# Kernel optimization log

Measured on AMD Instinct MI355X. Metric: run time of the kernel, lower is better.

The kernel has to match this reference:

```python
import jax, jax.numpy as jnp
import numpy as np

N = 2000      # batch_size * num_rois
PS = 7        # pool_size
C = 256       # roi-align channels
HID = 1024    # head width
NC = 81       # num_classes (COCO incl. background)
EPS = 1e-3    # keras BatchNormalization default epsilon


def setup_inputs() -> dict:
    key = jax.random.key(0)
    ks = jax.random.split(key, 6)
    sc = lambda k, shape, s: jax.random.normal(k, shape, jnp.float32) * s
    return {
        "pooled_rois": jax.random.normal(ks[0], (N, PS, PS, C), jnp.float32),
        # 7x7 VALID conv on a 7x7 input == flattened dense: [PS*PS*C, HID]
        "w1": sc(ks[1], (PS * PS * C, HID), 0.01),
        "b1": jnp.zeros((HID,), jnp.float32),
        "gamma1": jnp.ones((HID,), jnp.float32),
        "beta1": jnp.zeros((HID,), jnp.float32),
        # 1x1 conv == dense [HID, HID]
        "w2": sc(ks[2], (HID, HID), 0.02),
        "b2": jnp.zeros((HID,), jnp.float32),
        "gamma2": jnp.ones((HID,), jnp.float32),
        "beta2": jnp.zeros((HID,), jnp.float32),
        "w_logits": sc(ks[3], (HID, NC), 0.02),
        "b_logits": jnp.zeros((NC,), jnp.float32),
        "w_delta": sc(ks[4], (HID, NC * 4), 0.02),
        "b_delta": jnp.zeros((NC * 4,), jnp.float32),
    }


def _batchnorm_train(x, gamma, beta):
    # training=True: normalize with batch statistics over the RoI axis
    mu = jnp.mean(x, axis=0)
    var = jnp.var(x, axis=0)
    return gamma * (x - mu) * jax.lax.rsqrt(var + EPS) + beta


def reference(pooled_rois, w1, b1, gamma1, beta1, w2, b2, gamma2, beta2,
              w_logits, b_logits, w_delta, b_delta):
    n = pooled_rois.shape[0]
    # rcnn_class_conv1: 7x7 VALID conv on 7x7 input -> flatten + matmul
    x = pooled_rois.reshape(n, -1) @ w1 + b1          # [N, 1024]
    x = jax.nn.relu(_batchnorm_train(x, gamma1, beta1))
    # rcnn_class_conv2: 1x1 conv -> matmul
    x = x @ w2 + b2                                    # [N, 1024]
    x = jax.nn.relu(_batchnorm_train(x, gamma2, beta2))
    logits = x @ w_logits + b_logits                   # [N, NC]
    probs = jax.nn.softmax(logits, axis=-1)            # [N, NC]
    deltas = (x @ w_delta + b_delta).reshape(n, NC, 4) # [N, NC, 4]
    return logits, probs, deltas
```

## Files before the change

### kernel.cpp

```cpp
#include <hip/hip_runtime.h>

typedef unsigned short u16;
typedef __bf16 bf16x8 __attribute__((ext_vector_type(8)));
typedef float f32x4 __attribute__((ext_vector_type(4)));
typedef u16 u16x8 __attribute__((ext_vector_type(8)));

static constexpr int kNRoi = 2000;
static constexpr int kMPad = 2048;
static constexpr int kKin  = 12544;
static constexpr int kHid  = 1024;
static constexpr int kNOutPad = 512;
static constexpr int kNC = 81;
static constexpr int kND = 324;


__device__ __forceinline__ u16 f2bf(float f) {
  union { float f; unsigned u; } v; v.f = f;
  unsigned r = v.u + 0x7fffu + ((v.u >> 16) & 1u);
  return (u16)(r >> 16);
}

__device__ __forceinline__ void transpose64(const float* __restrict__ in,
                                            u16* __restrict__ out, int R, int C,
                                            int bx, int by, u16* t, int tid) {
  const int cb = bx * 64, rb = by * 64;
  const int rl = tid >> 4, cl = (tid & 15) * 4;
#pragma unroll
  for (int i = 0; i < 4; ++i) {
    int r = rl + i * 16;
    f32x4 v = *(const f32x4*)(in + (long)(rb + r) * C + cb + cl);
#pragma unroll
    for (int j = 0; j < 4; ++j) t[(cl + j) * 72 + r] = f2bf(v[j]);
  }
  __syncthreads();
  const int c2 = tid >> 3, r2 = (tid & 7) * 8;
#pragma unroll
  for (int i = 0; i < 2; ++i) {
    int c = c2 + i * 32;
    u16x8 v = *(const u16x8*)&t[c * 72 + r2];
    *(u16x8*)(out + (long)(cb + c) * R + rb + r2) = v;
  }
}

__device__ __forceinline__ void transpose32(const float* __restrict__ in,
                                            u16* __restrict__ out, int R, int C,
                                            int bx, int by, u16* t, int tid) {
  int tx = tid & 31, ty = tid >> 5;
  int cb = bx * 32, rb = by * 32;
#pragma unroll
  for (int i = 0; i < 4; ++i) {
    int r = rb + ty + i * 8, c = cb + tx;
    if (r < R && c < C) t[(ty + i * 8) * 33 + tx] = f2bf(in[(long)r * C + c]);
  }
  __syncthreads();
#pragma unroll
  for (int i = 0; i < 4; ++i) {
    int c = cb + ty + i * 8, r = rb + tx;
    if (c < C && r < R) out[(long)c * R + r] = t[tx * 33 + ty + i * 8];
  }
}

__global__ __launch_bounds__(256) void prep(
    const float* __restrict__ w1, const float* __restrict__ w2,
    const float* __restrict__ wl, const float* __restrict__ wd,
    u16* __restrict__ W1T, u16* __restrict__ W2T, u16* __restrict__ WHT,
    float* __restrict__ S) {
  __shared__ u16 sh[64 * 72];
  const int tid = threadIdx.x;
  int id = blockIdx.x;
  if (id < 3136) { transpose64(w1, W1T, kKin, kHid, id & 15, id >> 4, sh, tid); return; }
  id -= 3136;
  if (id < 256)  { transpose64(w2, W2T, kHid, kHid, id & 15, id >> 4, sh, tid); return; }
  id -= 256;
  if (id < 96)   { transpose32(wl, WHT, kHid, kNC, id % 3, id / 3, sh, tid); return; }
  id -= 96;
  if (id < 352)  { transpose32(wd, WHT + kNC * kHid, kHid, kND, id % 11, id / 11, sh, tid); return; }
  id -= 352;
  if (id < 54) {
    int idx = id * 256 + tid;
    if (idx < 13696) *(u16x8*)(WHT + 405 * kHid + idx * 8) = (u16x8){};
    return;
  }
  id -= 54;
  *(f32x4*)(S + ((long)id * 256 + tid) * 4) = (f32x4){};
}

template<int AF32>
__global__ __launch_bounds__(256, 2) void gemm128(
    const float* __restrict__ Af, const u16* __restrict__ Ah,
    const u16* __restrict__ Bt, float* __restrict__ Cz, long zstride,
    int Mreal, int K, int N, int gy, int ntPer) {
  __shared__ u16 As[2][8192];
  __shared__ u16 Bs[2][8192];
  const int tid  = threadIdx.x;
  const int lane = tid & 63;
  const int w    = tid >> 6;
  const int wm   = (w >> 1) * 64;
  const int wn   = (w & 1) * 64;

  const int bl  = blockIdx.x;
  const int s   = bl >> 3;
  const int bx  = (bl & 7) * 2 + (s & 1);
  const int t2  = s >> 1;
  const int by  = t2 % gy;
  const int z   = t2 / gy;
  const long kb = (long)z * ntPer * 64;
  const int NT  = ntPer;

  const int rS = w * 8 + (lane >> 3);
  const int sg = (lane & 7) ^ ((lane >> 3) & 7);
  const u16* bp[4];
#pragma unroll
  for (int j = 0; j < 4; ++j)
    bp[j] = Bt + (long)(by * 128 + rS + j * 32) * K + kb + sg * 8;

  const u16* ap[4];
  const float* afp = nullptr;
  int rw = 0, hw = 0;
  if (AF32) {
    rw = tid >> 1; hw = tid & 1;
    long arow = (long)bx * 128 + rw; if (arow > Mreal - 1) arow = Mreal - 1;
    afp = Af + arow * K + kb + hw * 32;
  } else {
#pragma unroll
    for (int j = 0; j < 4; ++j) {
      long arow = (long)bx * 128 + rS + j * 32; if (arow > Mreal - 1) arow = Mreal - 1;
      ap[j] = Ah + arow * K + kb + sg * 8;
    }
  }

#define GLDS(p, dst) __builtin_amdgcn_global_load_lds( \
    (const __attribute__((address_space(1))) void*)(p), \
    (__attribute__((address_space(3))) void*)(dst), 16, 0, 0)
#define STG_B(b) do { _Pragma("unroll") for (int j_ = 0; j_ < 4; ++j_) { \
    GLDS(bp[j_], &Bs[b][j_ * 2048 + w * 512]); bp[j_] += 64; } } while (0)
#define STG_A(b) do { _Pragma("unroll") for (int j_ = 0; j_ < 4; ++j_) { \
    GLDS(ap[j_], &As[b][j_ * 2048 + w * 512]); ap[j_] += 64; } } while (0)

  f32x4 ar[8];
#define LDA32 do { _Pragma("unroll") for (int j_ = 0; j_ < 8; ++j_) \
    ar[j_] = *(const f32x4*)(afp + j_ * 4); afp += 64; } while (0)
#define WRA(b) do { _Pragma("unroll") for (int k_ = 0; k_ < 4; ++k_) { \
    u16x8 hh; _Pragma("unroll") for (int e_ = 0; e_ < 4; ++e_) { \
      hh[e_] = f2bf(ar[2 * k_][e_]); hh[4 + e_] = f2bf(ar[2 * k_ + 1][e_]); } \
    *(u16x8*)(&As[b][rw * 64 + ((hw * 4 + k_) ^ (rw & 7)) * 8]) = hh; } } while (0)

  const int fr = lane & 15;
  const int q  = lane >> 4;
  const int g0 = (q ^ (fr & 7)) * 8;
  const int g1 = ((q + 4) ^ (fr & 7)) * 8;

  f32x4 acc[4][4] = {};

#define LDFRAG(dst, base, off, gg) do { _Pragma("unroll") for (int i_ = 0; i_ < 4; ++i_) \
    dst[i_] = *(const bf16x8*)((base) + ((off) + i_ * 16 + fr) * 64 + (gg)); } while (0)
#define MM16(aa, bb) do { __builtin_amdgcn_s_setprio(1); \
    _Pragma("unroll") for (int mi_ = 0; mi_ < 4; ++mi_) \
    _Pragma("unroll") for (int ni_ = 0; ni_ < 4; ++ni_) \
      acc[mi_][ni_] = __builtin_amdgcn_mfma_f32_16x16x32_bf16( \
          aa[mi_], bb[ni_], acc[mi_][ni_], 0, 0, 0); \
    __builtin_amdgcn_s_setprio(0); } while (0)

  if (AF32) {
    LDA32;
    STG_B(0);
    asm volatile("s_waitcnt vmcnt(4)" ::: "memory");
    WRA(0);
  } else {
    STG_A(0); STG_B(0);
  }

  int cur = 0;
  for (int t = 0; t < NT; ++t) {
    const int nb = cur ^ 1;
    const bool more = (t + 1 < NT);
    if (more) {
      if (AF32) { LDA32; } else { STG_A(nb); }
      STG_B(nb);
      if (AF32) asm volatile("s_waitcnt vmcnt(12)" ::: "memory");
      else      asm volatile("s_waitcnt vmcnt(8)"  ::: "memory");
    } else {
      asm volatile("s_waitcnt vmcnt(0)" ::: "memory");
    }
    __builtin_amdgcn_s_barrier();
    __builtin_amdgcn_sched_barrier(0);

    const u16* as_ = As[cur];
    const u16* bs_ = Bs[cur];
    bf16x8 a0[4], b0[4], a1[4], b1[4];
    LDFRAG(a0, as_, wm, g0); LDFRAG(b0, bs_, wn, g0);
    MM16(a0, b0);
    LDFRAG(a1, as_, wm, g1); LDFRAG(b1, bs_, wn, g1);
    MM16(a1, b1);

    if (more && AF32) {
      asm volatile("s_waitcnt vmcnt(4)" ::: "memory");
      WRA(nb);
      asm volatile("s_waitcnt lgkmcnt(0)" ::: "memory");
    }
    __builtin_amdgcn_s_barrier();
    cur = nb;
  }
#undef GLDS
#undef STG_A
#undef STG_B
#undef LDA32
#undef WRA
#undef LDFRAG
#undef MM16

  float* Cw = Cz + (long)z * zstride;
  const int row0 = bx * 128 + wm + q * 4;
  const int col0 = by * 128 + wn + fr;
#pragma unroll
  for (int mi = 0; mi < 4; ++mi)
#pragma unroll
    for (int ni = 0; ni < 4; ++ni)
#pragma unroll
      for (int e = 0; e < 4; ++e)
        Cw[(long)(row0 + mi * 16 + e) * N + col0 + ni * 16] = acc[mi][ni][e];
}

__global__ __launch_bounds__(256) void reduce_stats(
    const float* __restrict__ Cz, float* __restrict__ X,
    float* __restrict__ S, float* __restrict__ SS, int nz) {
  const int col = (blockIdx.x & 3) * 256 + threadIdx.x;
  const int r0 = (blockIdx.x >> 2) * 32;
  float s = 0.f, ss = 0.f;
  for (int r = r0; r < r0 + 32; ++r) {
    float x = 0.f;
    for (int zz = 0; zz < nz; ++zz)
      x += Cz[((long)zz * kMPad + r) * kHid + col];
    X[(long)r * kHid + col] = x;
    if (r < kNRoi) { s += x; ss += x * x; }
  }
  atomicAdd(&S[col], s);
  atomicAdd(&SS[col], ss);
}

__global__ __launch_bounds__(256) void bn_relu(
    const float* __restrict__ X, const float* __restrict__ S,
    const float* __restrict__ SS, const float* __restrict__ gamma,
    const float* __restrict__ beta, u16* __restrict__ H) {
  constexpr float invN = 1.f / (float)kNRoi;
  long i = ((long)blockIdx.x * 256 + threadIdx.x) * 8;
  int c = (int)(i & (kHid - 1));
  f32x4 x0 = *(const f32x4*)(X + i);
  f32x4 x1 = *(const f32x4*)(X + i + 4);
  f32x4 s0 = *(const f32x4*)(S + c),    s1 = *(const f32x4*)(S + c + 4);
  f32x4 q0 = *(const f32x4*)(SS + c),   q1 = *(const f32x4*)(SS + c + 4);
  f32x4 g0 = *(const f32x4*)(gamma + c), g1 = *(const f32x4*)(gamma + c + 4);
  f32x4 b0 = *(const f32x4*)(beta + c),  b1 = *(const f32x4*)(beta + c + 4);
  u16x8 h;
#pragma unroll
  for (int j = 0; j < 4; ++j) {
    float mu = s0[j] * invN;
    float var = q0[j] * invN - mu * mu;
    float sc = g0[j] * rsqrtf(var + 1e-3f);
    h[j] = f2bf(fmaxf(0.f, sc * x0[j] + (b0[j] - mu * sc)));
    mu = s1[j] * invN;
    var = q1[j] * invN - mu * mu;
    sc = g1[j] * rsqrtf(var + 1e-3f);
    h[4 + j] = f2bf(fmaxf(0.f, sc * x1[j] + (b1[j] - mu * sc)));
  }
  *(u16x8*)(H + i) = h;
}

__device__ __forceinline__ float rd8(const float* __restrict__ xr, int c) {
  float v = 0.f;
#pragma unroll
  for (int z = 0; z < 8; ++z) v += xr[(long)z * kMPad * kNOutPad + c];
  return v;
}

__global__ __launch_bounds__(256) void head_out(
    const float* __restrict__ Xz, const float* __restrict__ bl,
    const float* __restrict__ bd, float* __restrict__ out) {
  int lane = threadIdx.x & 63;
  int row = blockIdx.x * 4 + (threadIdx.x >> 6);
  if (row >= kNRoi) return;
  const float* xr = Xz + (long)row * kNOutPad;
  float v0 = rd8(xr, lane) + bl[lane];
  float v1 = (lane < kNC - 64) ? rd8(xr, 64 + lane) + bl[64 + lane] : -3.0e38f;
  float m = fmaxf(v0, v1);
#pragma unroll
  for (int off = 32; off > 0; off >>= 1) m = fmaxf(m, __shfl_xor(m, off, 64));
  float e0 = __expf(v0 - m);
  float e1 = (lane < kNC - 64) ? __expf(v1 - m) : 0.f;
  float s = e0 + e1;
#pragma unroll
  for (int off = 32; off > 0; off >>= 1) s += __shfl_xor(s, off, 64);
  float inv = 1.f / s;
  float* lo = out + (long)row * kNC;
  float* pr = out + (long)kNRoi * kNC + (long)row * kNC;
  float* de = out + 2L * kNRoi * kNC + (long)row * kND;
  lo[lane] = v0;
  pr[lane] = e0 * inv;
  if (lane < kNC - 64) { lo[64 + lane] = v1; pr[64 + lane] = e1 * inv; }
#pragma unroll
  for (int j = 0; j < 5; ++j) {
    int c = lane + 64 * j;
    de[c] = rd8(xr, kNC + c) + bd[c];
  }
  if (lane < 4) { int c = lane + 320; de[c] = rd8(xr, kNC + c) + bd[c]; }
}

extern "C" void kernel_launch(void* const* d_in, const int* in_sizes, int n_in,
                              void* d_out, int out_size, void* d_ws, size_t ws_size,
                              hipStream_t stream) {
  const float* pooled   = (const float*)d_in[0];
  const float* w1       = (const float*)d_in[1];
  const float* gamma1   = (const float*)d_in[3];
  const float* beta1    = (const float*)d_in[4];
  const float* w2       = (const float*)d_in[5];
  const float* gamma2   = (const float*)d_in[7];
  const float* beta2    = (const float*)d_in[8];
  const float* w_logits = (const float*)d_in[9];
  const float* b_logits = (const float*)d_in[10];
  const float* w_delta  = (const float*)d_in[11];
  const float* b_delta  = (const float*)d_in[12];

  char* ws = (char*)d_ws;
  u16*   W1T = (u16*)(ws + 0);
  u16*   W2T = (u16*)(ws + 25690112);
  u16*   WHT = (u16*)(ws + 27787264);
  float* S   = (float*)(ws + 28835840);
  u16*   H   = (u16*)(ws + 28852224);
  float* X   = (float*)(ws + 33046528);
  float* Pz  = (float*)(ws + 41435136);

  float* S1  = S;
  float* SS1 = S + 1024;
  float* S2  = S + 2048;
  float* SS2 = S + 3072;

  prep<<<3898, 256, 0, stream>>>(w1, w2, w_logits, w_delta, W1T, W2T, WHT, S);

  gemm128<1><<<512, 256, 0, stream>>>(pooled, nullptr, W1T, Pz, 2048L * 1024,
                                      kNRoi, kKin, kHid, 8, 49);

  reduce_stats<<<256, 256, 0, stream>>>(Pz, X, S1, SS1, 4);
  bn_relu<<<(kMPad * kHid) / 2048, 256, 0, stream>>>(X, S1, SS1, gamma1, beta1, H);

  gemm128<0><<<512, 256, 0, stream>>>(nullptr, H, W2T, Pz, 2048L * 1024,
                                      kMPad, kHid, kHid, 8, 4);

  reduce_stats<<<256, 256, 0, stream>>>(Pz, X, S2, SS2, 4);
  bn_relu<<<(kMPad * kHid) / 2048, 256, 0, stream>>>(X, S2, SS2, gamma2, beta2, H);

  gemm128<0><<<512, 256, 0, stream>>>(nullptr, H, WHT, Pz, 2048L * 512,
                                      kMPad, kHid, kNOutPad, 4, 2);

  head_out<<<kNRoi / 4, 256, 0, stream>>>(Pz, b_logits, b_delta, (float*)d_out);
}
```

Measured before the change: 440.9 us.

## Fuse whole RCNN head into one persistent kernel with grid barriers

Replaces the eight separate launches with one persistent 256-block kernel that uses a software grid barrier between phases. It pre-converts the pooled input to bf16 instead of converting fp32 inside the GEMM loop. It switches GEMM1 to 256x256 tiles with an 8-way split-K reduced by atomicAdd into a zeroed buffer. The intent is to remove launch overhead, inter-kernel gaps and the separate reduce pass. The cost is a spin-wait barrier that relies on all 256 blocks being co-resident, atomic contention on X, and an extra bf16 copy of the input in the workspace.

```diff
diff --git a/kernel.cpp b/kernel.cpp
--- a/kernel.cpp
+++ b/kernel.cpp
@@ -14,204 +14,171 @@
 static constexpr int kND = 324;
 
 
+__device__ unsigned g_cnt = 0;
+__device__ unsigned g_gen = 0;
+
+__device__ __forceinline__ void gsync() {
+  __syncthreads();
+  if (threadIdx.x == 0) {
+    __threadfence();
+    unsigned my = atomicAdd(&g_gen, 0u);
+    unsigned n = atomicAdd(&g_cnt, 1u) + 1;
+    if (n == 256u) {
+      atomicExch(&g_cnt, 0u);
+      __threadfence();
+      atomicAdd(&g_gen, 1u);
+    } else {
+      while (atomicAdd(&g_gen, 0u) == my) {}
+    }
+    __threadfence();
+  }
+  __syncthreads();
+}
+
 __device__ __forceinline__ u16 f2bf(float f) {
   union { float f; unsigned u; } v; v.f = f;
   unsigned r = v.u + 0x7fffu + ((v.u >> 16) & 1u);
   return (u16)(r >> 16);
 }
 
-__device__ __forceinline__ void transpose64(const float* __restrict__ in,
-                                            u16* __restrict__ out, int R, int C,
-                                            int bx, int by, u16* t, int tid) {
-  const int cb = bx * 64, rb = by * 64;
-  const int rl = tid >> 4, cl = (tid & 15) * 4;
-#pragma unroll
-  for (int i = 0; i < 4; ++i) {
-    int r = rl + i * 16;
-    f32x4 v = *(const f32x4*)(in + (long)(rb + r) * C + cb + cl);
-#pragma unroll
-    for (int j = 0; j < 4; ++j) t[(cl + j) * 72 + r] = f2bf(v[j]);
-  }
-  __syncthreads();
-  const int c2 = tid >> 3, r2 = (tid & 7) * 8;
-#pragma unroll
-  for (int i = 0; i < 2; ++i) {
-    int c = c2 + i * 32;
-    u16x8 v = *(const u16x8*)&t[c * 72 + r2];
-    *(u16x8*)(out + (long)(cb + c) * R + rb + r2) = v;
-  }
-}
-
-__device__ __forceinline__ void transpose32(const float* __restrict__ in,
-                                            u16* __restrict__ out, int R, int C,
-                                            int bx, int by, u16* t, int tid) {
-  int tx = tid & 31, ty = tid >> 5;
-  int cb = bx * 32, rb = by * 32;
-#pragma unroll
-  for (int i = 0; i < 4; ++i) {
-    int r = rb + ty + i * 8, c = cb + tx;
-    if (r < R && c < C) t[(ty + i * 8) * 33 + tx] = f2bf(in[(long)r * C + c]);
-  }
-  __syncthreads();
-#pragma unroll
-  for (int i = 0; i < 4; ++i) {
-    int c = cb + ty + i * 8, r = rb + tx;
-    if (c < C && r < R) out[(long)c * R + r] = t[tx * 33 + ty + i * 8];
-  }
-}
-
-__global__ __launch_bounds__(256) void prep(
-    const float* __restrict__ w1, const float* __restrict__ w2,
-    const float* __restrict__ wl, const float* __restrict__ wd,
-    u16* __restrict__ W1T, u16* __restrict__ W2T, u16* __restrict__ WHT,
-    float* __restrict__ S) {
-  __shared__ u16 sh[64 * 72];
-  const int tid = threadIdx.x;
-  int id = blockIdx.x;
-  if (id < 3136) { transpose64(w1, W1T, kKin, kHid, id & 15, id >> 4, sh, tid); return; }
-  id -= 3136;
-  if (id < 256)  { transpose64(w2, W2T, kHid, kHid, id & 15, id >> 4, sh, tid); return; }
-  id -= 256;
-  if (id < 96)   { transpose32(wl, WHT, kHid, kNC, id % 3, id / 3, sh, tid); return; }
-  id -= 96;
-  if (id < 352)  { transpose32(wd, WHT + kNC * kHid, kHid, kND, id % 11, id / 11, sh, tid); return; }
-  id -= 352;
-  if (id < 54) {
-    int idx = id * 256 + tid;
-    if (idx < 13696) *(u16x8*)(WHT + 405 * kHid + idx * 8) = (u16x8){};
-    return;
-  }
-  id -= 54;
-  *(f32x4*)(S + ((long)id * 256 + tid) * 4) = (f32x4){};
-}
-
-template<int AF32>
-__global__ __launch_bounds__(256, 2) void gemm128(
-    const float* __restrict__ Af, const u16* __restrict__ Ah,
-    const u16* __restrict__ Bt, float* __restrict__ Cz, long zstride,
-    int Mreal, int K, int N, int gy, int ntPer) {
-  __shared__ u16 As[2][8192];
-  __shared__ u16 Bs[2][8192];
-  const int tid  = threadIdx.x;
-  const int lane = tid & 63;
-  const int w    = tid >> 6;
-  const int wm   = (w >> 1) * 64;
-  const int wn   = (w & 1) * 64;
-
-  const int bl  = blockIdx.x;
-  const int s   = bl >> 3;
-  const int bx  = (bl & 7) * 2 + (s & 1);
-  const int t2  = s >> 1;
-  const int by  = t2 % gy;
-  const int z   = t2 / gy;
-  const long kb = (long)z * ntPer * 64;
-  const int NT  = ntPer;
-
-  const int rS = w * 8 + (lane >> 3);
-  const int sg = (lane & 7) ^ ((lane >> 3) & 7);
-  const u16* bp[4];
+#define GLDS(p, d) __builtin_amdgcn_global_load_lds( \
+    (const __attribute__((address_space(1))) void*)(p), \
+    (__attribute__((address_space(3))) void*)(d), 16, 0, 0)
+
+__device__ __forceinline__ void tr64(const float* __restrict__ src,
+                                     u16* __restrict__ dst, int R,
+                                     int cb, int rb, u16* t, int tid) {
+  const int rl = tid >> 3, cl = (tid & 7) * 8;
+  f32x4 v0 = *(const f32x4*)(src + (long)(rb + rl) * 1024 + cb + cl);
+  f32x4 v1 = *(const f32x4*)(src + (long)(rb + rl) * 1024 + cb + cl + 4);
+#pragma unroll
+  for (int j = 0; j < 4; ++j) {
+    t[(cl + j) * 72 + rl] = f2bf(v0[j]);
+    t[(cl + 4 + j) * 72 + rl] = f2bf(v1[j]);
+  }
+  __syncthreads();
+  *(u16x8*)(dst + (long)(cb + rl) * R + rb + cl) = *(const u16x8*)&t[rl * 72 + cl];
+  __syncthreads();
+}
+
+__device__ __forceinline__ void tr32(const float* __restrict__ src,
+                                     u16* __restrict__ dst, int srcC,
+                                     int cb, int rb, u16* t, int tid) {
+  const int tx = tid & 31, ty = tid >> 5;
+#pragma unroll
+  for (int j = 0; j < 2; ++j) {
+    int r = rb + ty + j * 16, c = cb + tx;
+    if (c < srcC) t[(ty + j * 16) * 33 + tx] = f2bf(src[(long)r * srcC + c]);
+  }
+  __syncthreads();
+#pragma unroll
+  for (int j = 0; j < 2; ++j) {
+    int c = cb + ty + j * 16, r = rb + tx;
+    if (c < srcC) dst[(long)c * 1024 + r] = t[tx * 33 + ty + j * 16];
+  }
+  __syncthreads();
+}
+
+__device__ __forceinline__ void bn_phase(const float* __restrict__ X,
+    const float* __restrict__ Sv, const float* __restrict__ SSv,
+    const float* __restrict__ gamma, const float* __restrict__ beta,
+    u16* __restrict__ H, int g) {
+  constexpr float invN = 1.f / (float)kNRoi;
+#pragma unroll
+  for (int h2 = 0; h2 < 2; ++h2) {
+    long i = (long)g * 16 + h2 * 8;
+    int c = (int)(i & (kHid - 1));
+    f32x4 x0 = *(const f32x4*)(X + i);
+    f32x4 x1 = *(const f32x4*)(X + i + 4);
+    f32x4 s0 = *(const f32x4*)(Sv + c),    s1 = *(const f32x4*)(Sv + c + 4);
+    f32x4 q0 = *(const f32x4*)(SSv + c),   q1 = *(const f32x4*)(SSv + c + 4);
+    f32x4 g0 = *(const f32x4*)(gamma + c), g1 = *(const f32x4*)(gamma + c + 4);
+    f32x4 b0 = *(const f32x4*)(beta + c),  b1 = *(const f32x4*)(beta + c + 4);
+    u16x8 h;
+#pragma unroll
+    for (int j = 0; j < 4; ++j) {
+      float mu = s0[j] * invN;
+      float var = q0[j] * invN - mu * mu;
+      float sc = g0[j] * rsqrtf(var + 1e-3f);
+      h[j] = f2bf(fmaxf(0.f, sc * x0[j] + (b0[j] - mu * sc)));
+      mu = s1[j] * invN;
+      var = q1[j] * invN - mu * mu;
+      sc = g1[j] * rsqrtf(var + 1e-3f);
+      h[4 + j] = f2bf(fmaxf(0.f, sc * x1[j] + (b1[j] - mu * sc)));
+    }
+    *(u16x8*)(H + i) = h;
+  }
+}
+
+__device__ __forceinline__ void gemm_bn128(
+    const u16* __restrict__ Ab, const u16* __restrict__ Btb,
+    float* __restrict__ Cw, int bxm, int byn, int kb, int NT, int N,
+    u16 (*Asb)[16384], u16 (*Bsb)[16384], int tid) {
+  const int lane = tid & 63, w = tid >> 6;
+  const int wm = (w >> 1) * 64, wn = (w & 1) * 64;
+  const int rS = tid >> 3;
+  const int sg = (tid & 7) ^ (rS & 7);
+  const u16* aq[4]; const u16* bq[2];
 #pragma unroll
   for (int j = 0; j < 4; ++j)
-    bp[j] = Bt + (long)(by * 128 + rS + j * 32) * K + kb + sg * 8;
-
-  const u16* ap[4];
-  const float* afp = nullptr;
-  int rw = 0, hw = 0;
-  if (AF32) {
-    rw = tid >> 1; hw = tid & 1;
-    long arow = (long)bx * 128 + rw; if (arow > Mreal - 1) arow = Mreal - 1;
-    afp = Af + arow * K + kb + hw * 32;
-  } else {
-#pragma unroll
-    for (int j = 0; j < 4; ++j) {
-      long arow = (long)bx * 128 + rS + j * 32; if (arow > Mreal - 1) arow = Mreal - 1;
-      ap[j] = Ah + arow * K + kb + sg * 8;
-    }
-  }
-
-#define GLDS(p, dst) __builtin_amdgcn_global_load_lds( \
-    (const __attribute__((address_space(1))) void*)(p), \
-    (__attribute__((address_space(3))) void*)(dst), 16, 0, 0)
-#define STG_B(b) do { _Pragma("unroll") for (int j_ = 0; j_ < 4; ++j_) { \
-    GLDS(bp[j_], &Bs[b][j_ * 2048 + w * 512]); bp[j_] += 64; } } while (0)
-#define STG_A(b) do { _Pragma("unroll") for (int j_ = 0; j_ < 4; ++j_) { \
-    GLDS(ap[j_], &As[b][j_ * 2048 + w * 512]); ap[j_] += 64; } } while (0)
-
-  f32x4 ar[8];
-#define LDA32 do { _Pragma("unroll") for (int j_ = 0; j_ < 8; ++j_) \
-    ar[j_] = *(const f32x4*)(afp + j_ * 4); afp += 64; } while (0)
-#define WRA(b) do { _Pragma("unroll") for (int k_ = 0; k_ < 4; ++k_) { \
-    u16x8 hh; _Pragma("unroll") for (int e_ = 0; e_ < 4; ++e_) { \
-      hh[e_] = f2bf(ar[2 * k_][e_]); hh[4 + e_] = f2bf(ar[2 * k_ + 1][e_]); } \
-    *(u16x8*)(&As[b][rw * 64 + ((hw * 4 + k_) ^ (rw & 7)) * 8]) = hh; } } while (0)
-
-  const int fr = lane & 15;
-  const int q  = lane >> 4;
-  const int g0 = (q ^ (fr & 7)) * 8;
-  const int g1 = ((q + 4) ^ (fr & 7)) * 8;
-
+    aq[j] = Ab + (long)(bxm * 256 + rS + j * 64) * 1024 + kb + sg * 8;
+#pragma unroll
+  for (int j = 0; j < 2; ++j)
+    bq[j] = Btb + (long)(byn * 128 + rS + j * 64) * 1024 + kb + sg * 8;
+
+#define STAGE2(b) do { _Pragma("unroll") for (int j_ = 0; j_ < 4; ++j_) { \
+      GLDS(aq[j_], &Asb[b][w * 512 + j_ * 4096]); aq[j_] += 64; } \
+    _Pragma("unroll") for (int j_ = 0; j_ < 2; ++j_) { \
+      GLDS(bq[j_], &Bsb[b][w * 512 + j_ * 4096]); bq[j_] += 64; } } while (0)
+
+  const int fr = lane & 15, q = lane >> 4;
+  const int g0 = (q ^ (fr & 7)) * 8, g1 = ((4 + q) ^ (fr & 7)) * 8;
   f32x4 acc[4][4] = {};
 
-#define LDFRAG(dst, base, off, gg) do { _Pragma("unroll") for (int i_ = 0; i_ < 4; ++i_) \
-    dst[i_] = *(const bf16x8*)((base) + ((off) + i_ * 16 + fr) * 64 + (gg)); } while (0)
-#define MM16(aa, bb) do { __builtin_amdgcn_s_setprio(1); \
-    _Pragma("unroll") for (int mi_ = 0; mi_ < 4; ++mi_) \
-    _Pragma("unroll") for (int ni_ = 0; ni_ < 4; ++ni_) \
-      acc[mi_][ni_] = __builtin_amdgcn_mfma_f32_16x16x32_bf16( \
-          aa[mi_], bb[ni_], acc[mi_][ni_], 0, 0, 0); \
-    __builtin_amdgcn_s_setprio(0); } while (0)
-
-  if (AF32) {
-    LDA32;
-    STG_B(0);
-    asm volatile("s_waitcnt vmcnt(4)" ::: "memory");
-    WRA(0);
-  } else {
-    STG_A(0); STG_B(0);
-  }
-
+  STAGE2(0);
   int cur = 0;
   for (int t = 0; t < NT; ++t) {
     const int nb = cur ^ 1;
     const bool more = (t + 1 < NT);
+    __builtin_amdgcn_s_barrier();
     if (more) {
-      if (AF32) { LDA32; } else { STG_A(nb); }
-      STG_B(nb);
-      if (AF32) asm volatile("s_waitcnt vmcnt(12)" ::: "memory");
-      else      asm volatile("s_waitcnt vmcnt(8)"  ::: "memory");
+      STAGE2(nb);
+      asm volatile("s_waitcnt vmcnt(6)" ::: "memory");
     } else {
       asm volatile("s_waitcnt vmcnt(0)" ::: "memory");
     }
     __builtin_amdgcn_s_barrier();
     __builtin_amdgcn_sched_barrier(0);
-
-    const u16* as_ = As[cur];
-    const u16* bs_ = Bs[cur];
+    const u16* as_ = Asb[cur];
+    const u16* bs_ = Bsb[cur];
     bf16x8 a0[4], b0[4], a1[4], b1[4];
-    LDFRAG(a0, as_, wm, g0); LDFRAG(b0, bs_, wn, g0);
-    MM16(a0, b0);
-    LDFRAG(a1, as_, wm, g1); LDFRAG(b1, bs_, wn, g1);
-    MM16(a1, b1);
-
-    if (more && AF32) {
-      asm volatile("s_waitcnt vmcnt(4)" ::: "memory");
-      WRA(nb);
-      asm volatile("s_waitcnt lgkmcnt(0)" ::: "memory");
-    }
-    __builtin_amdgcn_s_barrier();
+#pragma unroll
+    for (int i = 0; i < 4; ++i) a0[i] = *(const bf16x8*)(as_ + (wm + i * 16 + fr) * 64 + g0);
+#pragma unroll
+    for (int i = 0; i < 4; ++i) b0[i] = *(const bf16x8*)(bs_ + (wn + i * 16 + fr) * 64 + g0);
+    __builtin_amdgcn_s_setprio(1);
+#pragma unroll
+    for (int mi = 0; mi < 4; ++mi)
+#pragma unroll
+      for (int ni = 0; ni < 4; ++ni)
+        acc[mi][ni] = __builtin_amdgcn_mfma_f32_16x16x32_bf16(a0[mi], b0[ni], acc[mi][ni], 0, 0, 0);
+    __builtin_amdgcn_s_setprio(0);
+#pragma unroll
+    for (int i = 0; i < 4; ++i) a1[i] = *(const bf16x8*)(as_ + (wm + i * 16 + fr) * 64 + g1);
+#pragma unroll
+    for (int i = 0; i < 4; ++i) b1[i] = *(const bf16x8*)(bs_ + (wn + i * 16 + fr) * 64 + g1);
+    __builtin_amdgcn_s_setprio(1);
+#pragma unroll
+    for (int mi = 0; mi < 4; ++mi)
+#pragma unroll
+      for (int ni = 0; ni < 4; ++ni)
+        acc[mi][ni] = __builtin_amdgcn_mfma_f32_16x16x32_bf16(a1[mi], b1[ni], acc[mi][ni], 0, 0, 0);
+    __builtin_amdgcn_s_setprio(0);
     cur = nb;
   }
-#undef GLDS
-#undef STG_A
-#undef STG_B
-#undef LDA32
-#undef WRA
-#undef LDFRAG
-#undef MM16
-
-  float* Cw = Cz + (long)z * zstride;
-  const int row0 = bx * 128 + wm + q * 4;
-  const int col0 = by * 128 + wn + fr;
+#undef STAGE2
+  const int row0 = bxm * 256 + wm + q * 4;
+  const int col0 = byn * 128 + wn + fr;
 #pragma unroll
   for (int mi = 0; mi < 4; ++mi)
 #pragma unroll
@@ -221,93 +188,230 @@
         Cw[(long)(row0 + mi * 16 + e) * N + col0 + ni * 16] = acc[mi][ni][e];
 }
 
-__global__ __launch_bounds__(256) void reduce_stats(
-    const float* __restrict__ Cz, float* __restrict__ X,
-    float* __restrict__ S, float* __restrict__ SS, int nz) {
-  const int col = (blockIdx.x & 3) * 256 + threadIdx.x;
-  const int r0 = (blockIdx.x >> 2) * 32;
-  float s = 0.f, ss = 0.f;
-  for (int r = r0; r < r0 + 32; ++r) {
-    float x = 0.f;
-    for (int zz = 0; zz < nz; ++zz)
-      x += Cz[((long)zz * kMPad + r) * kHid + col];
-    X[(long)r * kHid + col] = x;
-    if (r < kNRoi) { s += x; ss += x * x; }
-  }
-  atomicAdd(&S[col], s);
-  atomicAdd(&SS[col], ss);
-}
-
-__global__ __launch_bounds__(256) void bn_relu(
-    const float* __restrict__ X, const float* __restrict__ S,
-    const float* __restrict__ SS, const float* __restrict__ gamma,
-    const float* __restrict__ beta, u16* __restrict__ H) {
-  constexpr float invN = 1.f / (float)kNRoi;
-  long i = ((long)blockIdx.x * 256 + threadIdx.x) * 8;
-  int c = (int)(i & (kHid - 1));
-  f32x4 x0 = *(const f32x4*)(X + i);
-  f32x4 x1 = *(const f32x4*)(X + i + 4);
-  f32x4 s0 = *(const f32x4*)(S + c),    s1 = *(const f32x4*)(S + c + 4);
-  f32x4 q0 = *(const f32x4*)(SS + c),   q1 = *(const f32x4*)(SS + c + 4);
-  f32x4 g0 = *(const f32x4*)(gamma + c), g1 = *(const f32x4*)(gamma + c + 4);
-  f32x4 b0 = *(const f32x4*)(beta + c),  b1 = *(const f32x4*)(beta + c + 4);
-  u16x8 h;
-#pragma unroll
-  for (int j = 0; j < 4; ++j) {
-    float mu = s0[j] * invN;
-    float var = q0[j] * invN - mu * mu;
-    float sc = g0[j] * rsqrtf(var + 1e-3f);
-    h[j] = f2bf(fmaxf(0.f, sc * x0[j] + (b0[j] - mu * sc)));
-    mu = s1[j] * invN;
-    var = q1[j] * invN - mu * mu;
-    sc = g1[j] * rsqrtf(var + 1e-3f);
-    h[4 + j] = f2bf(fmaxf(0.f, sc * x1[j] + (b1[j] - mu * sc)));
-  }
-  *(u16x8*)(H + i) = h;
-}
-
-__device__ __forceinline__ float rd8(const float* __restrict__ xr, int c) {
-  float v = 0.f;
-#pragma unroll
-  for (int z = 0; z < 8; ++z) v += xr[(long)z * kMPad * kNOutPad + c];
-  return v;
-}
-
-__global__ __launch_bounds__(256) void head_out(
-    const float* __restrict__ Xz, const float* __restrict__ bl,
-    const float* __restrict__ bd, float* __restrict__ out) {
-  int lane = threadIdx.x & 63;
-  int row = blockIdx.x * 4 + (threadIdx.x >> 6);
-  if (row >= kNRoi) return;
-  const float* xr = Xz + (long)row * kNOutPad;
-  float v0 = rd8(xr, lane) + bl[lane];
-  float v1 = (lane < kNC - 64) ? rd8(xr, 64 + lane) + bl[64 + lane] : -3.0e38f;
-  float m = fmaxf(v0, v1);
-#pragma unroll
-  for (int off = 32; off > 0; off >>= 1) m = fmaxf(m, __shfl_xor(m, off, 64));
-  float e0 = __expf(v0 - m);
-  float e1 = (lane < kNC - 64) ? __expf(v1 - m) : 0.f;
-  float s = e0 + e1;
-#pragma unroll
-  for (int off = 32; off > 0; off >>= 1) s += __shfl_xor(s, off, 64);
-  float inv = 1.f / s;
-  float* lo = out + (long)row * kNC;
-  float* pr = out + (long)kNRoi * kNC + (long)row * kNC;
-  float* de = out + 2L * kNRoi * kNC + (long)row * kND;
-  lo[lane] = v0;
-  pr[lane] = e0 * inv;
-  if (lane < kNC - 64) { lo[64 + lane] = v1; pr[64 + lane] = e1 * inv; }
-#pragma unroll
-  for (int j = 0; j < 5; ++j) {
-    int c = lane + 64 * j;
-    de[c] = rd8(xr, kNC + c) + bd[c];
-  }
-  if (lane < 4) { int c = lane + 320; de[c] = rd8(xr, kNC + c) + bd[c]; }
+__global__ __launch_bounds__(512, 2) void mega(
+    const float* __restrict__ pooled, const float* __restrict__ w1,
+    const float* __restrict__ w2, const float* __restrict__ wl,
+    const float* __restrict__ wd, const float* __restrict__ gamma1,
+    const float* __restrict__ beta1, const float* __restrict__ gamma2,
+    const float* __restrict__ beta2, const float* __restrict__ blg,
+    const float* __restrict__ bdl, u16* __restrict__ A1,
+    u16* __restrict__ W1T, u16* __restrict__ W2T, u16* __restrict__ WHT,
+    float* __restrict__ X, float* __restrict__ S, u16* __restrict__ H,
+    float* __restrict__ Pz, float* __restrict__ out) {
+  __shared__ u16 As[2][16384];
+  __shared__ u16 Bs[2][16384];
+  const int tid = threadIdx.x;
+  const int bl = blockIdx.x;
+  const int g = bl * 512 + tid;
+  const int lane = tid & 63;
+  const int w = tid >> 6;
+  float* S1 = S; float* SS1 = S + 1024; float* S2 = S + 2048; float* SS2 = S + 3072;
+
+  for (long i = (long)g * 8; i < 25088000L; i += 131072L * 8) {
+    f32x4 a = *(const f32x4*)(pooled + i);
+    f32x4 b = *(const f32x4*)(pooled + i + 4);
+    u16x8 h;
+#pragma unroll
+    for (int j = 0; j < 4; ++j) { h[j] = f2bf(a[j]); h[4 + j] = f2bf(b[j]); }
+    *(u16x8*)(A1 + i) = h;
+  }
+  {
+    u16* t = As[0];
+    for (int it = 0; it < 13; ++it) {
+      int tt = bl + it * 256;
+      if (tt < 3136) tr64(w1, W1T, kKin, (tt & 15) * 64, (tt >> 4) * 64, t, tid);
+    }
+    tr64(w2, W2T, kHid, (bl & 15) * 64, (bl >> 4) * 64, t, tid);
+    for (int it = 0; it < 2; ++it) {
+      int tt = bl + it * 256;
+      if (tt < 96) tr32(wl, WHT, kNC, (tt % 3) * 32, (tt / 3) * 32, t, tid);
+      else if (tt < 448) {
+        int u = tt - 96;
+        tr32(wd, WHT + kNC * kHid, kND, (u % 11) * 32, (u / 11) * 32, t, tid);
+      }
+    }
+  }
+  if (g < 13696) *(u16x8*)(WHT + 405 * kHid + (long)g * 8) = (u16x8){};
+  if (g < 1024)  *(f32x4*)(S + g * 4) = (f32x4){};
+#pragma unroll
+  for (int k = 0; k < 4; ++k)
+    *(f32x4*)(X + ((long)(g + k * 131072)) * 4) = (f32x4){};
+  gsync();
+
+  {
+    const int z  = bl & 7;
+    const int bx = (bl >> 3) & 7;
+    const int by = bl >> 6;
+    const int NT = 24 + (z < 4 ? 1 : 0);
+    const long kb = (long)(z * 24 + (z < 4 ? z : 4)) * 64;
+    const int wm = (w >> 2) * 128;
+    const int wn = (w & 3) * 64;
+    const int rA = w * 8 + (lane >> 3);
+    const int cgs = (lane & 7) ^ (rA & 7);
+    const u16* ap[4]; const u16* bp[4];
+#pragma unroll
+    for (int j = 0; j < 4; ++j) {
+      long arow = (long)bx * 256 + rA + j * 64; if (arow > kNRoi - 1) arow = kNRoi - 1;
+      ap[j] = A1 + arow * kKin + kb + cgs * 8;
+      bp[j] = W1T + (long)(by * 256 + rA + j * 64) * kKin + kb + cgs * 8;
+    }
+#define STAGE1(b) do { _Pragma("unroll") for (int j_ = 0; j_ < 4; ++j_) { \
+      GLDS(ap[j_], &As[b][w * 512 + j_ * 4096]); ap[j_] += 64; \
+      GLDS(bp[j_], &Bs[b][w * 512 + j_ * 4096]); bp[j_] += 64; } } while (0)
+    const int fr = lane & 15, q = lane >> 4;
+    const int g0 = (q ^ (fr & 7)) * 8, g1 = ((4 + q) ^ (fr & 7)) * 8;
+    f32x4 acc[8][4] = {};
+    STAGE1(0);
+    int cur = 0;
+    for (int t = 0; t < NT; ++t) {
+      const int nb = cur ^ 1;
+      const bool more = (t + 1 < NT);
+      __builtin_amdgcn_s_barrier();
+      if (more) {
+        STAGE1(nb);
+        asm volatile("s_waitcnt vmcnt(8)" ::: "memory");
+      } else {
+        asm volatile("s_waitcnt vmcnt(0)" ::: "memory");
+      }
+      __builtin_amdgcn_s_barrier();
+      __builtin_amdgcn_sched_barrier(0);
+      const u16* as_ = As[cur];
+      const u16* bs_ = Bs[cur];
+      bf16x8 a0[8], b0[4], a1[8], b1[4];
+#pragma unroll
+      for (int i = 0; i < 8; ++i) a0[i] = *(const bf16x8*)(as_ + (wm + i * 16 + fr) * 64 + g0);
+#pragma unroll
+      for (int i = 0; i < 4; ++i) b0[i] = *(const bf16x8*)(bs_ + (wn + i * 16 + fr) * 64 + g0);
+      __builtin_amdgcn_s_setprio(1);
+#pragma unroll
+      for (int mi = 0; mi < 8; ++mi)
+#pragma unroll
+        for (int ni = 0; ni < 4; ++ni)
+          acc[mi][ni] = __builtin_amdgcn_mfma_f32_16x16x32_bf16(a0[mi], b0[ni], acc[mi][ni], 0, 0, 0);
+      __builtin_amdgcn_s_setprio(0);
+#pragma unroll
+      for (int i = 0; i < 8; ++i) a1[i] = *(const bf16x8*)(as_ + (wm + i * 16 + fr) * 64 + g1);
+#pragma unroll
+      for (int i = 0; i < 4; ++i) b1[i] = *(const bf16x8*)(bs_ + (wn + i * 16 + fr) * 64 + g1);
+      __builtin_amdgcn_s_setprio(1);
+#pragma unroll
+      for (int mi = 0; mi < 8; ++mi)
+#pragma unroll
+        for (int ni = 0; ni < 4; ++ni)
+          acc[mi][ni] = __builtin_amdgcn_mfma_f32_16x16x32_bf16(a1[mi], b1[ni], acc[mi][ni], 0, 0, 0);
+      __builtin_amdgcn_s_setprio(0);
+      cur = nb;
+    }
+#undef STAGE1
+    const int row0 = bx * 256 + wm + q * 4;
+    const int col0 = by * 256 + wn + fr;
+#pragma unroll
+    for (int mi = 0; mi < 8; ++mi)
+#pragma unroll
+      for (int ni = 0; ni < 4; ++ni)
+#pragma unroll
+        for (int e = 0; e < 4; ++e)
+          atomicAdd(&X[(long)(row0 + mi * 16 + e) * kHid + col0 + ni * 16], acc[mi][ni][e]);
+  }
+  gsync();
+
+  {
+    const int col = g & 1023;
+    const int r0 = (g >> 10) * 16;
+    float s = 0.f, ss = 0.f;
+    for (int r = r0; r < r0 + 16; ++r)
+      if (r < kNRoi) { float x = X[(long)r * kHid + col]; s += x; ss += x * x; }
+    atomicAdd(&S1[col], s); atomicAdd(&SS1[col], ss);
+  }
+  gsync();
+
+  bn_phase(X, S1, SS1, gamma1, beta1, H, g);
+  gsync();
+
+  {
+    const int z = bl & 3, tile = bl >> 2;
+    gemm_bn128(H, W2T, Pz + (long)z * 2097152L, tile & 7, tile >> 3,
+               z * 256, 4, kHid, As, Bs, tid);
+  }
+  gsync();
+
+  {
+    const int col = g & 1023;
+    const int r0 = (g >> 10) * 16;
+    float s = 0.f, ss = 0.f;
+    for (int r = r0; r < r0 + 16; ++r) {
+      float x = 0.f;
+#pragma unroll
+      for (int zz = 0; zz < 4; ++zz)
+        x += Pz[(long)zz * 2097152L + (long)r * kHid + col];
+      X[(long)r * kHid + col] = x;
+      if (r < kNRoi) { s += x; ss += x * x; }
+    }
+    atomicAdd(&S2[col], s); atomicAdd(&SS2[col], ss);
+  }
+  gsync();
+
+  bn_phase(X, S2, SS2, gamma2, beta2, H, g);
+  gsync();
+
+  {
+    const int z = bl & 7, tile = bl >> 3;
+    gemm_bn128(H, WHT, Pz + (long)z * 1048576L, tile & 7, tile >> 3,
+               z * 128, 2, kNOutPad, As, Bs, tid);
+  }
+  gsync();
+
+  {
+    const int row = bl * 8 + w;
+    if (row < kNRoi) {
+      const float* xr = Pz + (long)row * kNOutPad;
+      float v0 = 0.f, v1 = 0.f;
+#pragma unroll
+      for (int z = 0; z < 8; ++z) v0 += xr[(long)z * 1048576L + lane];
+      v0 += blg[lane];
+      if (lane < kNC - 64) {
+#pragma unroll
+        for (int z = 0; z < 8; ++z) v1 += xr[(long)z * 1048576L + 64 + lane];
+        v1 += blg[64 + lane];
+      } else v1 = -3.0e38f;
+      float m = fmaxf(v0, v1);
+#pragma unroll
+      for (int off = 32; off > 0; off >>= 1) m = fmaxf(m, __shfl_xor(m, off, 64));
+      float e0 = __expf(v0 - m);
+      float e1 = (lane < kNC - 64) ? __expf(v1 - m) : 0.f;
+      float s = e0 + e1;
+#pragma unroll
+      for (int off = 32; off > 0; off >>= 1) s += __shfl_xor(s, off, 64);
+      float inv = 1.f / s;
+      float* lo = out + (long)row * kNC;
+      float* pr = out + (long)kNRoi * kNC + (long)row * kNC;
+      float* de = out + 2L * kNRoi * kNC + (long)row * kND;
+      lo[lane] = v0;
+      pr[lane] = e0 * inv;
+      if (lane < kNC - 64) { lo[64 + lane] = v1; pr[64 + lane] = e1 * inv; }
+#pragma unroll
+      for (int j = 0; j < 5; ++j) {
+        int c = lane + 64 * j;
+        float d = 0.f;
+#pragma unroll
+        for (int z = 0; z < 8; ++z) d += xr[(long)z * 1048576L + kNC + c];
+        de[c] = d + bdl[c];
+      }
+      if (lane < 4) {
+        int c = lane + 320;
+        float d = 0.f;
+#pragma unroll
+        for (int z = 0; z < 8; ++z) d += xr[(long)z * 1048576L + kNC + c];
+        de[c] = d + bdl[c];
+      }
+    }
+  }
 }
 
 extern "C" void kernel_launch(void* const* d_in, const int* in_sizes, int n_in,
                               void* d_out, int out_size, void* d_ws, size_t ws_size,
                               hipStream_t stream) {
+  (void)in_sizes; (void)n_in; (void)out_size; (void)ws_size;
   const float* pooled   = (const float*)d_in[0];
   const float* w1       = (const float*)d_in[1];
   const float* gamma1   = (const float*)d_in[3];
@@ -327,29 +431,11 @@
   float* S   = (float*)(ws + 28835840);
   u16*   H   = (u16*)(ws + 28852224);
   float* X   = (float*)(ws + 33046528);
+  u16*   A1  = (u16*)(ws + 41435136);
   float* Pz  = (float*)(ws + 41435136);
 
-  float* S1  = S;
-  float* SS1 = S + 1024;
-  float* S2  = S + 2048;
-  float* SS2 = S + 3072;
-
-  prep<<<3898, 256, 0, stream>>>(w1, w2, w_logits, w_delta, W1T, W2T, WHT, S);
-
-  gemm128<1><<<512, 256, 0, stream>>>(pooled, nullptr, W1T, Pz, 2048L * 1024,
-                                      kNRoi, kKin, kHid, 8, 49);
-
-  reduce_stats<<<256, 256, 0, stream>>>(Pz, X, S1, SS1, 4);
-  bn_relu<<<(kMPad * kHid) / 2048, 256, 0, stream>>>(X, S1, SS1, gamma1, beta1, H);
-
-  gemm128<0><<<512, 256, 0, stream>>>(nullptr, H, W2T, Pz, 2048L * 1024,
-                                      kMPad, kHid, kHid, 8, 4);
-
-  reduce_stats<<<256, 256, 0, stream>>>(Pz, X, S2, SS2, 4);
-  bn_relu<<<(kMPad * kHid) / 2048, 256, 0, stream>>>(X, S2, SS2, gamma2, beta2, H);
-
-  gemm128<0><<<512, 256, 0, stream>>>(nullptr, H, WHT, Pz, 2048L * 512,
-                                      kMPad, kHid, kNOutPad, 4, 2);
-
-  head_out<<<kNRoi / 4, 256, 0, stream>>>(Pz, b_logits, b_delta, (float*)d_out);
-}
+  mega<<<256, 512, 0, stream>>>(pooled, w1, w2, w_logits, w_delta,
+                                gamma1, beta1, gamma2, beta2,
+                                b_logits, b_delta,
+                                A1, W1T, W2T, WHT, X, S, H, Pz, (float*)d_out);
+}
```

After: 589.9 us. +33.8%, slower.
